# Performance work log

Hardware: AMD Instinct MI355X
Metric: run time of the kernel (lower is better)

Reference implementation:

```python
import jax, jax.numpy as jnp
import numpy as np
import math

B, S, H, NH = 4, 1024, 1536, 24
DH = H // NH
BUCKETS = 256          # position_buckets
MAX_REL = 512          # max_relative_positions
ATT_SPAN = BUCKETS     # pos_ebd_size
SCALE_FACTOR = 3       # 1 (content) + c2p + p2c
LN_EPS = 1e-7


def _make_log_bucket(rel, bucket_size, max_position):
    # numpy port of make_log_bucket_position (used only to build inputs)
    sign = np.sign(rel)
    mid = bucket_size // 2
    abs_pos = np.where((rel < mid) & (rel > -mid), mid - 1, np.abs(rel)).astype(np.float64)
    log_pos = np.ceil(np.log(abs_pos / mid) / np.log((max_position - 1) / mid) * (mid - 1)) + mid
    bucket = np.where(abs_pos <= mid, rel.astype(np.float64), log_pos * sign)
    return bucket.astype(np.int64)


def setup_inputs() -> dict:
    key = jax.random.key(0)
    ks = jax.random.split(key, 8)
    s = 0.02
    hidden_states = jax.random.normal(ks[0], (B, S, H), jnp.float32)
    rel_embeddings = jax.random.normal(ks[1], (2 * ATT_SPAN, H), jnp.float32)
    ids = np.arange(S)
    relative_pos = jnp.asarray(
        _make_log_bucket(ids[:, None] - ids[None, :], BUCKETS, MAX_REL)[None].astype(np.int32))  # [1,S,S]
    lengths = np.full((B,), S)
    lengths[B // 2:] = (3 * S) // 4  # some padded sequences
    valid = np.arange(S)[None, :] < lengths[:, None]  # [B,S]
    attention_mask = jnp.asarray(
        (valid[:, None, :, None] & valid[:, None, None, :]).astype(np.int32))  # [B,1,S,S]
    Wq = jax.random.normal(ks[2], (H, H), jnp.float32) * s
    Wk = jax.random.normal(ks[3], (H, H), jnp.float32) * s
    Wv = jax.random.normal(ks[4], (H, H), jnp.float32) * s
    Wo = jax.random.normal(ks[5], (H, H), jnp.float32) * s
    z = jnp.zeros((H,), jnp.float32)
    return dict(hidden_states=hidden_states, rel_embeddings=rel_embeddings,
                Wq=Wq, bq=z, Wk=Wk, bk=z, Wv=Wv, bv=z, Wo=Wo, bo=z,
                ln_g=jnp.ones((H,), jnp.float32), ln_b=z,
                attention_mask=attention_mask, relative_pos=relative_pos)


def _attention(hidden_states, rel_embeddings, Wq, bq, Wk, bk, Wv, bv, Wo, bo,
               ln_g, ln_b, attention_mask, relative_pos):
    Bm, Sm, Hm = hidden_states.shape

    def heads(x):  # [B,S,H] -> [B,NH,S,DH]
        return x.reshape(Bm, Sm, NH, DH).transpose(0, 2, 1, 3)

    q = heads(hidden_states @ Wq + bq)
    k = heads(hidden_states @ Wk + bk)
    v = heads(hidden_states @ Wv + bv)

    scale = math.sqrt(DH * SCALE_FACTOR)
    scores = jnp.einsum('bhqd,bhkd->bhqk', q, k) / scale  # content-to-content

    # share_att_key=True: reuse query/key projections on rel embeddings
    pos_k = (rel_embeddings @ Wk + bk).reshape(2 * ATT_SPAN, NH, DH).transpose(1, 0, 2)  # [NH,2P,DH]
    pos_q = (rel_embeddings @ Wq + bq).reshape(2 * ATT_SPAN, NH, DH).transpose(1, 0, 2)

    # content -> position
    c2p = jnp.einsum('bhqd,hpd->bhqp', q, pos_k)  # [B,NH,S,2P]
    c2p_idx = jnp.clip(relative_pos + ATT_SPAN, 0, 2 * ATT_SPAN - 1)[:, None]  # [1,1,S,S]
    c2p = jnp.take_along_axis(c2p, jnp.broadcast_to(c2p_idx, (Bm, NH, Sm, Sm)), axis=-1)
    scores = scores + c2p / scale

    # position -> content
    p2c = jnp.einsum('bhkd,hpd->bhkp', k, pos_q)  # [B,NH,S,2P]
    p2c_idx = jnp.clip(-relative_pos + ATT_SPAN, 0, 2 * ATT_SPAN - 1)[:, None]
    p2c = jnp.take_along_axis(p2c, jnp.broadcast_to(p2c_idx, (Bm, NH, Sm, Sm)), axis=-1)
    scores = scores + jnp.swapaxes(p2c, -1, -2) / scale

    # XSoftmax: mask==0 -> -inf before softmax, 0 after
    m = attention_mask.astype(bool)
    neg = jnp.finfo(scores.dtype).min
    probs = jax.nn.softmax(jnp.where(m, scores, neg), axis=-1)
    probs = jnp.where(m, probs, jnp.zeros((), scores.dtype))

    ctx = jnp.einsum('bhqk,bhkd->bhqd', probs, v)
    ctx = ctx.transpose(0, 2, 1, 3).reshape(Bm, Sm, Hm)

    # DebertaV2SelfOutput: dense + residual + LayerNorm
    out = ctx @ Wo + bo + hidden_states
    mu = jnp.mean(out, axis=-1, keepdims=True)
    var = jnp.mean(jnp.square(out - mu), axis=-1, keepdims=True)
    return (out - mu) / jnp.sqrt(var + LN_EPS) * ln_g + ln_b


def reference(hidden_states, rel_embeddings, Wq, bq, Wk, bk, Wv, bv, Wo, bo,
              ln_g, ln_b, attention_mask, relative_pos):
    return _attention(hidden_states, rel_embeddings, Wq, bq, Wk, bk, Wv, bv,
                      Wo, bo, ln_g, ln_b, attention_mask, relative_pos)
```

## Files before the change

### kernel.cpp

```cpp
#include <hip/hip_runtime.h>
#include <hip/hip_bf16.h>

constexpr int Bc  = 4;
constexpr int Sc  = 1024;
constexpr int Hc  = 1536;
constexpr int NHc = 24;
constexpr int P2c = 512;
constexpr int MX  = Bc * Sc;
constexpr int MA  = MX + P2c;
constexpr int N3  = 3 * Hc;
constexpr float INV_SCALE = 0.07216878364870323f;

using f32x4  = __attribute__((ext_vector_type(4))) float;
using bf16x8 = __attribute__((ext_vector_type(8))) short;
using i32x4  = __attribute__((ext_vector_type(4))) int;
using u16x8  = __attribute__((ext_vector_type(8))) unsigned short;
using u16x4  = __attribute__((ext_vector_type(4))) unsigned short;
typedef unsigned short u16;

#define DEV __device__ __forceinline__

DEV float bf2f(u16 u) { return __uint_as_float(((unsigned)u) << 16); }
DEV u16   f2bf(float f) { return __builtin_bit_cast(unsigned short, __float2bfloat16(f)); }

#if defined(__has_builtin)
#if __has_builtin(__builtin_amdgcn_global_load_lds)
#define HAVE_GLL 1
#endif
#endif
#ifndef HAVE_GLL
#define HAVE_GLL 0
#endif

DEV void stage32(u16* lds, const u16* g, int ldk, int lane) {
#pragma unroll
  for (int c = 0; c < 4; ++c) {
    const int row   = c * 8 + (lane >> 3);
    const int gslot = (lane & 7) ^ (row & 7);
    const u16* gp = g + (size_t)row * ldk + gslot * 8;
#if HAVE_GLL
    __builtin_amdgcn_global_load_lds(
        (const __attribute__((address_space(1))) void*)gp,
        (__attribute__((address_space(3))) void*)(lds + c * 8 * 64),
        16, 0, 0);
#else
    i32x4 v = *(const i32x4*)gp;
    *(i32x4*)(lds + row * 64 + (lane & 7) * 8) = v;
#endif
  }
}

DEV bf16x8 ldsFrag(const u16* base, int row, int kh, int lhi) {
  const int idx = row * 64 + ((kh * 32 + lhi * 8) ^ ((row & 7) * 8));
  return *(const bf16x8*)(base + idx);
}

template <int MODE>
__global__ __launch_bounds__(256) void gemm128(
    const u16* __restrict__ A, const u16* __restrict__ Bt,
    const float* __restrict__ bias, const float* __restrict__ resid,
    u16* __restrict__ outb, float* __restrict__ outf, int ldo)
{
  __shared__ alignas(16) u16 As[128 * 64];
  __shared__ alignas(16) u16 Bs[128 * 64];
  const int tid = threadIdx.x, wid = tid >> 6, lane = tid & 63;
  const int wr = wid >> 1, wc = wid & 1;
  const int l15 = lane & 15, lhi = lane >> 4;
  const int m0 = blockIdx.y * 128, n0 = blockIdx.x * 128;

  f32x4 acc[4][4] = {};
#pragma unroll 1
  for (int kt = 0; kt < 24; ++kt) {
    const int k0 = kt * 64;
    stage32(As + wid * (32 * 64), A  + (size_t)(m0 + wid * 32) * 1536 + k0, 1536, lane);
    stage32(Bs + wid * (32 * 64), Bt + (size_t)(n0 + wid * 32) * 1536 + k0, 1536, lane);
    asm volatile("s_waitcnt vmcnt(0)" ::: "memory");
    __syncthreads();
#pragma unroll
    for (int kh = 0; kh < 2; ++kh) {
      bf16x8 af[4], bfv[4];
#pragma unroll
      for (int mt = 0; mt < 4; ++mt) af[mt]  = ldsFrag(As, wr * 64 + mt * 16 + l15, kh, lhi);
#pragma unroll
      for (int nt = 0; nt < 4; ++nt) bfv[nt] = ldsFrag(Bs, wc * 64 + nt * 16 + l15, kh, lhi);
#pragma unroll
      for (int mt = 0; mt < 4; ++mt)
#pragma unroll
        for (int nt = 0; nt < 4; ++nt)
          acc[mt][nt] = __builtin_amdgcn_mfma_f32_16x16x32_bf16(af[mt], bfv[nt], acc[mt][nt], 0, 0, 0);
    }
    __syncthreads();
  }
#pragma unroll
  for (int mt = 0; mt < 4; ++mt)
#pragma unroll
    for (int nt = 0; nt < 4; ++nt) {
      const int gn = n0 + wc * 64 + nt * 16 + l15;
      const float bs = bias[gn];
#pragma unroll
      for (int r = 0; r < 4; ++r) {
        const int gm = m0 + wr * 64 + mt * 16 + lhi * 4 + r;
        float v = acc[mt][nt][r] + bs;
        if (MODE == 0) {
          if (gn < Hc) v *= INV_SCALE;
          outb[(size_t)gm * ldo + gn] = f2bf(v);
        } else {
          v += resid[(size_t)gm * ldo + gn];
          outf[(size_t)gm * ldo + gn] = v;
        }
      }
    }
}

__global__ __launch_bounds__(256) void prep_misc(
    const float* __restrict__ bq, const float* __restrict__ bk, const float* __restrict__ bv,
    const int* __restrict__ am, const int* __restrict__ rp,
    float* __restrict__ bias, int* __restrict__ valid, u16* __restrict__ tbl)
{
  const int TOT = N3 + MX + 2047;
  for (int i = blockIdx.x * 256 + threadIdx.x; i < TOT; i += gridDim.x * 256) {
    if (i < N3) {
      bias[i] = i < Hc ? bq[i] : (i < 2 * Hc ? bk[i - Hc] : bv[i - 2 * Hc]);
    } else if (i < N3 + MX) {
      const int j = i - N3, b = j >> 10, s = j & 1023;
      valid[j] = am[(size_t)b * Sc * Sc + (size_t)s * Sc + s];
    } else {
      const int t = i - (N3 + MX), d = t - 1023;
      int v = (d >= 0 ? rp[(size_t)d * Sc] : rp[-d]) + 256;
      v = v < 0 ? 0 : (v > 511 ? 511 : v);
      tbl[t] = (u16)v;
    }
  }
}

__global__ void len_kernel(const int* __restrict__ valid, int* __restrict__ LENS)
{
  const int tid = threadIdx.x, wid = tid >> 6, lane = tid & 63;
  int s = 0;
#pragma unroll
  for (int j = 0; j < 16; ++j) s += valid[wid * Sc + j * 64 + lane];
#pragma unroll
  for (int off = 1; off <= 32; off <<= 1) s += __shfl_xor(s, off);
  if (lane == 0) LENS[wid] = s;
}

__global__ __launch_bounds__(256) void cast_x(const float* __restrict__ hs,
                                              const float* __restrict__ rel,
                                              u16* __restrict__ A)
{
  const size_t total = (size_t)MA * Hc / 4;
  for (size_t i = (size_t)blockIdx.x * 256 + threadIdx.x; i < total; i += (size_t)gridDim.x * 256) {
    const size_t e = i * 4;
    const int row = (int)(e / Hc), col = (int)(e % Hc);
    const float* s = row < MX ? hs + (size_t)row * Hc + col : rel + (size_t)(row - MX) * Hc + col;
    f32x4 v = *(const f32x4*)s;
    u16x4 o = { f2bf(v[0]), f2bf(v[1]), f2bf(v[2]), f2bf(v[3]) };
    *(u16x4*)(A + e) = o;
  }
}

__global__ void transpose_cast(const float* __restrict__ Wq, const float* __restrict__ Wk,
                               const float* __restrict__ Wv, const float* __restrict__ Wo,
                               u16* __restrict__ WT, u16* __restrict__ WOT)
{
  const int z = blockIdx.z;
  const float* src = z == 0 ? Wq : z == 1 ? Wk : z == 2 ? Wv : Wo;
  u16* dst = z == 3 ? WOT : WT + (size_t)z * Hc * Hc;
  __shared__ float t[32][33];
  const int tx = threadIdx.x, ty = threadIdx.y;
  const int kb = blockIdx.y * 32, nb = blockIdx.x * 32;
#pragma unroll
  for (int i = 0; i < 4; ++i)
    t[ty + i * 8][tx] = src[(size_t)(kb + ty + i * 8) * Hc + nb + tx];
  __syncthreads();
#pragma unroll
  for (int i = 0; i < 4; ++i)
    dst[(size_t)(nb + ty + i * 8) * Hc + kb + tx] = f2bf(t[tx][ty + i * 8]);
}

__global__ __launch_bounds__(256) void relmat3(const u16* __restrict__ QKVP,
    u16* __restrict__ c2p, u16* __restrict__ p2cT, int bh_base)
{
  const int z = blockIdx.y, lbh = z >> 1, var = z & 1;
  const int bh = bh_base + lbh, b = bh / NHc, h = bh % NHc;
  const int t = blockIdx.x;
  const int tid = threadIdx.x, wid = tid >> 6, lane = tid & 63;
  const int wr = wid >> 1, wc = wid & 1;
  const int l15 = lane & 15, lhi = lane >> 4;

  int m0, n0, ldo;
  size_t arowb, browb;
  u16* out;
  if (var == 0) {
    m0 = (t >> 2) * 64; n0 = (t & 3) * 128; ldo = P2c;
    arowb = (size_t)b * Sc + m0;  browb = (size_t)MX + n0;
    out = c2p + (size_t)lbh * Sc * P2c;
  } else {
    m0 = (t >> 3) * 64; n0 = (t & 7) * 128; ldo = Sc;
    arowb = (size_t)MX + m0;      browb = (size_t)b * Sc + n0;
    out = p2cT + (size_t)lbh * P2c * Sc;
  }
  const int acol = h * 64;
  const int bcol = Hc + h * 64;

  f32x4 acc[2][4] = {};
#pragma unroll
  for (int kh = 0; kh < 2; ++kh) {
    bf16x8 a[2], bb[4];
#pragma unroll
    for (int mt = 0; mt < 2; ++mt)
      a[mt] = *(const bf16x8*)(QKVP + (arowb + wr * 32 + mt * 16 + l15) * 4608
                               + acol + kh * 32 + lhi * 8);
#pragma unroll
    for (int nt = 0; nt < 4; ++nt)
      bb[nt] = *(const bf16x8*)(QKVP + (browb + wc * 64 + nt * 16 + l15) * 4608
                                + bcol + kh * 32 + lhi * 8);
#pragma unroll
    for (int mt = 0; mt < 2; ++mt)
#pragma unroll
      for (int nt = 0; nt < 4; ++nt)
        acc[mt][nt] = __builtin_amdgcn_mfma_f32_16x16x32_bf16(a[mt], bb[nt], acc[mt][nt], 0, 0, 0);
  }
#pragma unroll
  for (int mt = 0; mt < 2; ++mt)
#pragma unroll
    for (int nt = 0; nt < 4; ++nt)
#pragma unroll
      for (int r = 0; r < 4; ++r) {
        const int mm = m0 + wr * 32 + mt * 16 + (lhi << 2) + r;
        const int nn = n0 + wc * 64 + nt * 16 + l15;
        out[(size_t)mm * ldo + nn] = f2bf(acc[mt][nt][r]);
      }
}

DEV int svz(int d) { return ((d ^ (d >> 3)) & 7) << 3; }

__global__ __launch_bounds__(256) void flash4(
    const u16* __restrict__ QKVP, const u16* __restrict__ c2p, const u16* __restrict__ p2cT,
    const int* __restrict__ LENS, const u16* __restrict__ tblG,
    u16* __restrict__ ctx, int bh_base, int chunkC)
{
  int id = blockIdx.x;
  const int grid = chunkC * 16;
  if ((grid & 7) == 0) {
    const int cpx = grid >> 3;
    id = (id & 7) * cpx + (id >> 3);
  }
  const int lbh = id >> 4, qi = id & 15;
  const int bh = bh_base + lbh, b = bh / NHc, h = bh % NHc;
  const int tid = threadIdx.x, wid = tid >> 6, lane = tid & 63;
  const int l15 = lane & 15, lhi = lane >> 4, lhi4 = lhi * 4;
  const int qrb = qi * 64 + wid * 16;
  const int len = LENS[b], nkt = (len + 63) >> 6;

  __shared__ u16 Tt[2048];
  __shared__ alignas(16) u16 Kt[64 * 64];
  __shared__ alignas(16) u16 Vt[64 * 64];
  __shared__ alignas(16) u16 Pl[4][16 * 64];

  for (int i = tid; i < 2047; i += 256) Tt[i] = tblG[i];

  bf16x8 aq[2];
#pragma unroll
  for (int kh = 0; kh < 2; ++kh)
    aq[kh] = *(const bf16x8*)(QKVP + (size_t)(b * Sc + qrb + l15) * 4608 + h * 64 + kh * 32 + lhi * 8);

  const int kr = tid >> 2, dc = (tid & 3) * 16;
  const int sk = (kr & 7) * 8;
  const u16* Kg = QKVP + (size_t)b * Sc * 4608 + Hc + h * 64;
  const u16* Vg = QKVP + (size_t)b * Sc * 4608 + 2 * Hc + h * 64;

  auto writeKV = [&](u16x8 ka, u16x8 kb, u16x8 va, u16x8 vb) {
    *(u16x8*)(Kt + kr * 64 + (dc ^ sk))       = ka;
    *(u16x8*)(Kt + kr * 64 + ((dc ^ sk) ^ 8)) = kb;
#pragma unroll
    for (int i = 0; i < 8; ++i) { const int d = dc + i;     Vt[d * 64 + (kr ^ svz(d))] = va[i]; }
#pragma unroll
    for (int i = 0; i < 8; ++i) { const int d = dc + 8 + i; Vt[d * 64 + (kr ^ svz(d))] = vb[i]; }
  };

  {
    const size_t ro = (size_t)kr * 4608 + dc;
    u16x8 ka = *(const u16x8*)(Kg + ro), kb = *(const u16x8*)(Kg + ro + 8);
    u16x8 va = *(const u16x8*)(Vg + ro), vb = *(const u16x8*)(Vg + ro + 8);
    writeKV(ka, kb, va, vb);
  }
  __syncthreads();

  const u16* c2pB  = c2p  + (size_t)lbh * Sc * P2c;
  const u16* p2cTB = p2cT + (size_t)lbh * P2c * Sc;
  u16* myP = Pl[wid];
  f32x4 o_acc[4] = {};
  float m_arr[4], l_arr[4];
#pragma unroll
  for (int r = 0; r < 4; ++r) { m_arr[r] = -1e30f; l_arr[r] = 0.f; }

  for (int kt = 0; kt < nkt; ++kt) {
    const int k0 = kt * 64;
    const bool more = (kt + 1 < nkt);
    u16x8 nka, nkb, nva, nvb;
    if (more) {
      const size_t ro = (size_t)(k0 + 64 + kr) * 4608 + dc;
      nka = *(const u16x8*)(Kg + ro); nkb = *(const u16x8*)(Kg + ro + 8);
      nva = *(const u16x8*)(Vg + ro); nvb = *(const u16x8*)(Vg + ro + 8);
    }

    float relv[4][4];
#pragma unroll
    for (int j = 0; j < 4; ++j)
#pragma unroll
      for (int r = 0; r < 4; ++r) {
        const int q = qrb + lhi4 + r;
        const int k = k0 + j * 16 + l15;
        const int cc = Tt[q - k + 1023];
        relv[j][r] = bf2f(c2pB[(size_t)q * P2c + cc]) + bf2f(p2cTB[(size_t)cc * Sc + k]);
      }

    f32x4 s[4];
    __builtin_amdgcn_s_setprio(1);
#pragma unroll
    for (int j = 0; j < 4; ++j) {
      f32x4 sv = {};
#pragma unroll
      for (int kh = 0; kh < 2; ++kh) {
        bf16x8 bk = ldsFrag(Kt, j * 16 + l15, kh, lhi);
        sv = __builtin_amdgcn_mfma_f32_16x16x32_bf16(aq[kh], bk, sv, 0, 0, 0);
      }
      s[j] = sv;
    }
    __builtin_amdgcn_s_setprio(0);

    float p[4][4];
#pragma unroll
    for (int j = 0; j < 4; ++j) {
      const bool kv = (k0 + j * 16 + l15) < len;
#pragma unroll
      for (int r = 0; r < 4; ++r)
        p[j][r] = kv ? (s[j][r] + relv[j][r]) : -1e30f;
    }

    float resc[4];
#pragma unroll
    for (int r = 0; r < 4; ++r) {
      float mx = fmaxf(fmaxf(p[0][r], p[1][r]), fmaxf(p[2][r], p[3][r]));
#pragma unroll
      for (int off = 1; off <= 8; off <<= 1) mx = fmaxf(mx, __shfl_xor(mx, off));
      const float mnew = fmaxf(m_arr[r], mx);
      const float sc = __expf(m_arr[r] - mnew);
      float rs = 0.f;
#pragma unroll
      for (int j = 0; j < 4; ++j) { p[j][r] = __expf(p[j][r] - mnew); rs += p[j][r]; }
#pragma unroll
      for (int off = 1; off <= 8; off <<= 1) rs += __shfl_xor(rs, off);
      l_arr[r] = l_arr[r] * sc + rs;
      m_arr[r] = mnew;
      resc[r] = sc;
    }
#pragma unroll
    for (int jd = 0; jd < 4; ++jd)
#pragma unroll
      for (int r = 0; r < 4; ++r) o_acc[jd][r] *= resc[r];

#pragma unroll
    for (int j = 0; j < 4; ++j)
#pragma unroll
      for (int r = 0; r < 4; ++r) {
        const int row = lhi4 + r, col = j * 16 + l15;
        myP[row * 64 + (col ^ ((row & 7) * 8))] = f2bf(p[j][r]);
      }

    __builtin_amdgcn_s_setprio(1);
#pragma unroll
    for (int kh = 0; kh < 2; ++kh) {
      bf16x8 pa = *(const bf16x8*)(myP + l15 * 64 + ((kh * 32 + lhi * 8) ^ ((l15 & 7) * 8)));
#pragma unroll
      for (int jd = 0; jd < 4; ++jd) {
        const int d = jd * 16 + l15;
        bf16x8 vf = *(const bf16x8*)(Vt + d * 64 + ((kh * 32 + lhi * 8) ^ svz(d)));
        o_acc[jd] = __builtin_amdgcn_mfma_f32_16x16x32_bf16(pa, vf, o_acc[jd], 0, 0, 0);
      }
    }
    __builtin_amdgcn_s_setprio(0);

    __syncthreads();
    if (more) writeKV(nka, nkb, nva, nvb);
    __syncthreads();
  }

#pragma unroll
  for (int r = 0; r < 4; ++r) {
    const int q = qrb + lhi4 + r;
    const float inv = (q < len && l_arr[r] > 0.f) ? 1.f / l_arr[r] : 0.f;
#pragma unroll
    for (int jd = 0; jd < 4; ++jd)
      ctx[(size_t)(b * Sc + q) * Hc + h * 64 + jd * 16 + l15] = f2bf(o_acc[jd][r] * inv);
  }
}

__global__ __launch_bounds__(256) void ln_kernel(float* __restrict__ io,
    const float* __restrict__ g, const float* __restrict__ bta)
{
  const int row = blockIdx.x;
  float* p = io + (size_t)row * Hc;
  const int tid = threadIdx.x, wid = tid >> 6, lane = tid & 63;
  float v[6];
  float s = 0.f;
#pragma unroll
  for (int j = 0; j < 6; ++j) { v[j] = p[tid + j * 256]; s += v[j]; }
#pragma unroll
  for (int off = 1; off <= 32; off <<= 1) s += __shfl_xor(s, off);
  __shared__ float red[4];
  if (lane == 0) red[wid] = s;
  __syncthreads();
  const float mu = (red[0] + red[1] + red[2] + red[3]) * (1.f / Hc);
  float q = 0.f;
#pragma unroll
  for (int j = 0; j < 6; ++j) { const float d = v[j] - mu; q += d * d; }
#pragma unroll
  for (int off = 1; off <= 32; off <<= 1) q += __shfl_xor(q, off);
  __syncthreads();
  if (lane == 0) red[wid] = q;
  __syncthreads();
  const float rstd = rsqrtf((red[0] + red[1] + red[2] + red[3]) * (1.f / Hc) + 1e-7f);
#pragma unroll
  for (int j = 0; j < 6; ++j) {
    const int c = tid + j * 256;
    p[c] = (v[j] - mu) * rstd * g[c] + bta[c];
  }
}

extern "C" void kernel_launch(void* const* d_in, const int* in_sizes, int n_in,
                              void* d_out, int out_size, void* d_ws, size_t ws_size,
                              hipStream_t stream)
{
  (void)in_sizes; (void)n_in; (void)out_size;
  const float* hidden = (const float*)d_in[0];
  const float* relemb = (const float*)d_in[1];
  const float* Wq = (const float*)d_in[2];
  const float* bq = (const float*)d_in[3];
  const float* Wk = (const float*)d_in[4];
  const float* bk = (const float*)d_in[5];
  const float* Wv = (const float*)d_in[6];
  const float* bv = (const float*)d_in[7];
  const float* Wo = (const float*)d_in[8];
  const float* bo = (const float*)d_in[9];
  const float* lng = (const float*)d_in[10];
  const float* lnb = (const float*)d_in[11];
  const int* am = (const int*)d_in[12];
  const int* rp = (const int*)d_in[13];
  float* out = (float*)d_out;

  char* ws = (char*)d_ws;
  size_t off = 0;
  auto alloc = [&](size_t bytes) { size_t r = off; off += (bytes + 255) & ~(size_t)255; return r; };
  const size_t o_qkvp = alloc((size_t)MA * 4608 * 2);
  const size_t o_wt   = alloc((size_t)N3 * Hc * 2);
  const size_t o_wot  = alloc((size_t)Hc * Hc * 2);
  const size_t o_abig = alloc((size_t)MA * Hc * 2);
  const size_t o_bias = alloc((size_t)N3 * 4);
  const size_t o_valid= alloc((size_t)MX * 4);
  const size_t o_tbl  = alloc(2048 * 2);
  const size_t o_lens = alloc(256);
  const size_t fixed  = off;
  const size_t o_rel  = off;

  const size_t perbh = (size_t)Sc * P2c * 2 * 2;
  int c = 96;
  while (c > 1 && fixed + (size_t)c * perbh > ws_size) c >>= 1;

  u16* QKVP = (u16*)(ws + o_qkvp);
  u16* WT   = (u16*)(ws + o_wt);
  u16* WOT  = (u16*)(ws + o_wot);
  u16* ABIG = (u16*)(ws + o_abig);
  u16* CTX  = (u16*)(ws + o_abig);
  float* BIAS = (float*)(ws + o_bias);
  int* VALID  = (int*)(ws + o_valid);
  u16* TBL  = (u16*)(ws + o_tbl);
  int* LENS = (int*)(ws + o_lens);
  u16* C2P  = (u16*)(ws + o_rel);
  u16* P2CT = C2P + (size_t)c * Sc * P2c;

  prep_misc<<<dim3(50), dim3(256), 0, stream>>>(bq, bk, bv, am, rp, BIAS, VALID, TBL);
  len_kernel<<<dim3(1), dim3(256), 0, stream>>>(VALID, LENS);
  cast_x<<<dim3(1728), dim3(256), 0, stream>>>(hidden, relemb, ABIG);
  transpose_cast<<<dim3(48, 48, 4), dim3(32, 8), 0, stream>>>(Wq, Wk, Wv, Wo, WT, WOT);
  gemm128<0><<<dim3(36, 36), dim3(256), 0, stream>>>(ABIG, WT, BIAS, (const float*)nullptr,
                                                     QKVP, (float*)nullptr, 4608);
  for (int base = 0; base < 96; base += c) {
    relmat3<<<dim3(64, 2 * c), dim3(256), 0, stream>>>(QKVP, C2P, P2CT, base);
    flash4<<<dim3(c * 16), dim3(256), 0, stream>>>(QKVP, C2P, P2CT, LENS, TBL, CTX, base, c);
  }
  gemm128<1><<<dim3(12, 32), dim3(256), 0, stream>>>(CTX, WOT, bo, hidden,
                                                     (u16*)nullptr, out, Hc);
  ln_kernel<<<dim3(MX), dim3(256), 0, stream>>>(out, lng, lnb);
}
```

Baseline: 450.5 us.

## Add double-buffered 256x192 QKV GEMM and prefetch relative-bias gathers in flash

Replaces the QKV projection GEMM with a 512-thread, 256x192-tile kernel. It double-buffers LDS and interleaves global-to-LDS staging of the next K-slice with the MFMA work on the current one, and it remaps blocks for L2 locality. The aim is to hide the load latency that the old version exposed with a full vmcnt(0) wait and barrier every K step. The flash attention kernel now prefetches the next tile's c2p/p2c gathered bias values into registers during the current tile, so those scattered loads are off the critical path. The cost is higher register pressure and larger LDS use, which may limit occupancy.

```diff
diff --git a/kernel.cpp b/kernel.cpp
--- a/kernel.cpp
+++ b/kernel.cpp
@@ -22,6 +22,7 @@
 
 DEV float bf2f(u16 u) { return __uint_as_float(((unsigned)u) << 16); }
 DEV u16   f2bf(float f) { return __builtin_bit_cast(unsigned short, __float2bfloat16(f)); }
+DEV void  bar() { __builtin_amdgcn_s_barrier(); asm volatile("" ::: "memory"); }
 
 #if defined(__has_builtin)
 #if __has_builtin(__builtin_amdgcn_global_load_lds)
@@ -55,11 +56,137 @@
   return *(const bf16x8*)(base + idx);
 }
 
-template <int MODE>
-__global__ __launch_bounds__(256) void gemm128(
+__global__ __launch_bounds__(512, 2) void gemm256k(
+    const u16* __restrict__ A, const u16* __restrict__ Bt,
+    const float* __restrict__ bias, u16* __restrict__ outb)
+{
+  constexpr int BM = 256, BN = 192;
+  __shared__ alignas(16) u16 As[2][BM * 64];
+  __shared__ alignas(16) u16 Bs[2][BN * 64];
+  const int tid = threadIdx.x, wid = tid >> 6, lane = tid & 63;
+  const int wr = wid >> 2, wc = wid & 3;
+  const int l15 = lane & 15, lhi = lane >> 4;
+
+  int id = blockIdx.x;
+  id = (id & 7) * 54 + (id >> 3);
+  const int m0 = (id / 24) * BM, n0 = (id % 24) * BN;
+
+  const int srow = tid >> 3;
+  const int gsl  = (tid & 7) ^ (srow & 7);
+
+  auto stageA = [&](int buf, int ck, int k0) {
+    const u16* gp = A + (size_t)(m0 + ck * 64 + srow) * 1536 + k0 + gsl * 8;
+#if HAVE_GLL
+    __builtin_amdgcn_global_load_lds(
+        (const __attribute__((address_space(1))) void*)gp,
+        (__attribute__((address_space(3))) void*)(&As[buf][ck * 4096 + wid * 512]),
+        16, 0, 0);
+#else
+    *(i32x4*)(&As[buf][ck * 4096 + srow * 64 + (tid & 7) * 8]) = *(const i32x4*)gp;
+#endif
+  };
+  auto stageB = [&](int buf, int ck, int k0) {
+    const u16* gp = Bt + (size_t)(n0 + ck * 64 + srow) * 1536 + k0 + gsl * 8;
+#if HAVE_GLL
+    __builtin_amdgcn_global_load_lds(
+        (const __attribute__((address_space(1))) void*)gp,
+        (__attribute__((address_space(3))) void*)(&Bs[buf][ck * 4096 + wid * 512]),
+        16, 0, 0);
+#else
+    *(i32x4*)(&Bs[buf][ck * 4096 + srow * 64 + (tid & 7) * 8]) = *(const i32x4*)gp;
+#endif
+  };
+
+  f32x4 acc[8][3] = {};
+
+  stageA(0, 0, 0); stageA(0, 1, 0); stageA(0, 2, 0); stageA(0, 3, 0);
+  stageB(0, 0, 0); stageB(0, 1, 0); stageB(0, 2, 0);
+
+  int cur = 0;
+#pragma unroll 1
+  for (int kt = 0; kt < 24; ++kt) {
+    const int nk0 = kt * 64 + 64;
+    const bool more = (kt < 23);
+    const int nb = cur ^ 1;
+
+    if (more) { stageA(nb, 0, nk0); stageA(nb, 1, nk0); }
+    if (more) asm volatile("s_waitcnt vmcnt(2)" ::: "memory");
+    else      asm volatile("s_waitcnt vmcnt(0)" ::: "memory");
+    bar();
+    bf16x8 bf[3], af[4];
+#pragma unroll
+    for (int nt = 0; nt < 3; ++nt) bf[nt] = ldsFrag(Bs[cur], wc * 48 + nt * 16 + l15, 0, lhi);
+#pragma unroll
+    for (int mt = 0; mt < 4; ++mt) af[mt] = ldsFrag(As[cur], wr * 128 + mt * 16 + l15, 0, lhi);
+    __builtin_amdgcn_s_setprio(1);
+#pragma unroll
+    for (int mt = 0; mt < 4; ++mt)
+#pragma unroll
+      for (int nt = 0; nt < 3; ++nt)
+        acc[mt][nt] = __builtin_amdgcn_mfma_f32_16x16x32_bf16(af[mt], bf[nt], acc[mt][nt], 0, 0, 0);
+    __builtin_amdgcn_s_setprio(0);
+    if (more) { stageA(nb, 2, nk0); stageA(nb, 3, nk0); }
+    bar();
+
+#pragma unroll
+    for (int mt = 0; mt < 4; ++mt) af[mt] = ldsFrag(As[cur], wr * 128 + 64 + mt * 16 + l15, 0, lhi);
+    __builtin_amdgcn_s_setprio(1);
+#pragma unroll
+    for (int mt = 0; mt < 4; ++mt)
+#pragma unroll
+      for (int nt = 0; nt < 3; ++nt)
+        acc[4 + mt][nt] = __builtin_amdgcn_mfma_f32_16x16x32_bf16(af[mt], bf[nt], acc[4 + mt][nt], 0, 0, 0);
+    __builtin_amdgcn_s_setprio(0);
+    if (more) { stageB(nb, 0, nk0); stageB(nb, 1, nk0); }
+    bar();
+
+#pragma unroll
+    for (int nt = 0; nt < 3; ++nt) bf[nt] = ldsFrag(Bs[cur], wc * 48 + nt * 16 + l15, 1, lhi);
+#pragma unroll
+    for (int mt = 0; mt < 4; ++mt) af[mt] = ldsFrag(As[cur], wr * 128 + mt * 16 + l15, 1, lhi);
+    __builtin_amdgcn_s_setprio(1);
+#pragma unroll
+    for (int mt = 0; mt < 4; ++mt)
+#pragma unroll
+      for (int nt = 0; nt < 3; ++nt)
+        acc[mt][nt] = __builtin_amdgcn_mfma_f32_16x16x32_bf16(af[mt], bf[nt], acc[mt][nt], 0, 0, 0);
+    __builtin_amdgcn_s_setprio(0);
+    if (more) { stageB(nb, 2, nk0); }
+    bar();
+
+#pragma unroll
+    for (int mt = 0; mt < 4; ++mt) af[mt] = ldsFrag(As[cur], wr * 128 + 64 + mt * 16 + l15, 1, lhi);
+    __builtin_amdgcn_s_setprio(1);
+#pragma unroll
+    for (int mt = 0; mt < 4; ++mt)
+#pragma unroll
+      for (int nt = 0; nt < 3; ++nt)
+        acc[4 + mt][nt] = __builtin_amdgcn_mfma_f32_16x16x32_bf16(af[mt], bf[nt], acc[4 + mt][nt], 0, 0, 0);
+    __builtin_amdgcn_s_setprio(0);
+    bar();
+
+    cur ^= 1;
+  }
+
+#pragma unroll
+  for (int mg = 0; mg < 8; ++mg)
+#pragma unroll
+    for (int nt = 0; nt < 3; ++nt) {
+      const int gn = n0 + wc * 48 + nt * 16 + l15;
+      const float bs = bias[gn];
+      const float sc = gn < Hc ? INV_SCALE : 1.f;
+#pragma unroll
+      for (int r = 0; r < 4; ++r) {
+        const int gm = m0 + wr * 128 + mg * 16 + (lhi << 2) + r;
+        outb[(size_t)gm * 4608 + gn] = f2bf((acc[mg][nt][r] + bs) * sc);
+      }
+    }
+}
+
+__global__ __launch_bounds__(256) void gemm128o(
     const u16* __restrict__ A, const u16* __restrict__ Bt,
     const float* __restrict__ bias, const float* __restrict__ resid,
-    u16* __restrict__ outb, float* __restrict__ outf, int ldo)
+    float* __restrict__ outf, int ldo)
 {
   __shared__ alignas(16) u16 As[128 * 64];
   __shared__ alignas(16) u16 Bs[128 * 64];
@@ -100,14 +227,7 @@
 #pragma unroll
       for (int r = 0; r < 4; ++r) {
         const int gm = m0 + wr * 64 + mt * 16 + lhi * 4 + r;
-        float v = acc[mt][nt][r] + bs;
-        if (MODE == 0) {
-          if (gn < Hc) v *= INV_SCALE;
-          outb[(size_t)gm * ldo + gn] = f2bf(v);
-        } else {
-          v += resid[(size_t)gm * ldo + gn];
-          outf[(size_t)gm * ldo + gn] = v;
-        }
+        outf[(size_t)gm * ldo + gn] = acc[mt][nt][r] + bs + resid[(size_t)gm * ldo + gn];
       }
     }
 }
@@ -235,7 +355,7 @@
 
 DEV int svz(int d) { return ((d ^ (d >> 3)) & 7) << 3; }
 
-__global__ __launch_bounds__(256) void flash4(
+__global__ __launch_bounds__(256) void flash5(
     const u16* __restrict__ QKVP, const u16* __restrict__ c2p, const u16* __restrict__ p2cT,
     const int* __restrict__ LENS, const u16* __restrict__ tblG,
     u16* __restrict__ ctx, int bh_base, int chunkC)
@@ -294,6 +414,18 @@
   float m_arr[4], l_arr[4];
 #pragma unroll
   for (int r = 0; r < 4; ++r) { m_arr[r] = -1e30f; l_arr[r] = 0.f; }
+
+  u16 rc[16], rp[16];
+#pragma unroll
+  for (int j = 0; j < 4; ++j)
+#pragma unroll
+    for (int r = 0; r < 4; ++r) {
+      const int q = qrb + lhi4 + r;
+      const int k = j * 16 + l15;
+      const int cc = Tt[q - k + 1023];
+      rc[j * 4 + r] = c2pB[(size_t)q * P2c + cc];
+      rp[j * 4 + r] = p2cTB[(size_t)cc * Sc + k];
+    }
 
   for (int kt = 0; kt < nkt; ++kt) {
     const int k0 = kt * 64;
@@ -304,17 +436,19 @@
       nka = *(const u16x8*)(Kg + ro); nkb = *(const u16x8*)(Kg + ro + 8);
       nva = *(const u16x8*)(Vg + ro); nvb = *(const u16x8*)(Vg + ro + 8);
     }
-
-    float relv[4][4];
-#pragma unroll
-    for (int j = 0; j < 4; ++j)
-#pragma unroll
-      for (int r = 0; r < 4; ++r) {
-        const int q = qrb + lhi4 + r;
-        const int k = k0 + j * 16 + l15;
-        const int cc = Tt[q - k + 1023];
-        relv[j][r] = bf2f(c2pB[(size_t)q * P2c + cc]) + bf2f(p2cTB[(size_t)cc * Sc + k]);
-      }
+    u16 nrc[16], nrp[16];
+    if (more) {
+#pragma unroll
+      for (int j = 0; j < 4; ++j)
+#pragma unroll
+        for (int r = 0; r < 4; ++r) {
+          const int q = qrb + lhi4 + r;
+          const int k = k0 + 64 + j * 16 + l15;
+          const int cc = Tt[q - k + 1023];
+          nrc[j * 4 + r] = c2pB[(size_t)q * P2c + cc];
+          nrp[j * 4 + r] = p2cTB[(size_t)cc * Sc + k];
+        }
+    }
 
     f32x4 s[4];
     __builtin_amdgcn_s_setprio(1);
@@ -336,7 +470,7 @@
       const bool kv = (k0 + j * 16 + l15) < len;
 #pragma unroll
       for (int r = 0; r < 4; ++r)
-        p[j][r] = kv ? (s[j][r] + relv[j][r]) : -1e30f;
+        p[j][r] = kv ? (s[j][r] + bf2f(rc[j * 4 + r]) + bf2f(rp[j * 4 + r])) : -1e30f;
     }
 
     float resc[4];
@@ -383,7 +517,11 @@
     __builtin_amdgcn_s_setprio(0);
 
     __syncthreads();
-    if (more) writeKV(nka, nkb, nva, nvb);
+    if (more) {
+      writeKV(nka, nkb, nva, nvb);
+#pragma unroll
+      for (int i = 0; i < 16; ++i) { rc[i] = nrc[i]; rp[i] = nrp[i]; }
+    }
     __syncthreads();
   }
 
@@ -484,13 +622,11 @@
   len_kernel<<<dim3(1), dim3(256), 0, stream>>>(VALID, LENS);
   cast_x<<<dim3(1728), dim3(256), 0, stream>>>(hidden, relemb, ABIG);
   transpose_cast<<<dim3(48, 48, 4), dim3(32, 8), 0, stream>>>(Wq, Wk, Wv, Wo, WT, WOT);
-  gemm128<0><<<dim3(36, 36), dim3(256), 0, stream>>>(ABIG, WT, BIAS, (const float*)nullptr,
-                                                     QKVP, (float*)nullptr, 4608);
+  gemm256k<<<dim3(432), dim3(512), 0, stream>>>(ABIG, WT, BIAS, QKVP);
   for (int base = 0; base < 96; base += c) {
     relmat3<<<dim3(64, 2 * c), dim3(256), 0, stream>>>(QKVP, C2P, P2CT, base);
-    flash4<<<dim3(c * 16), dim3(256), 0, stream>>>(QKVP, C2P, P2CT, LENS, TBL, CTX, base, c);
-  }
-  gemm128<1><<<dim3(12, 32), dim3(256), 0, stream>>>(CTX, WOT, bo, hidden,
-                                                     (u16*)nullptr, out, Hc);
+    flash5<<<dim3(c * 16), dim3(256), 0, stream>>>(QKVP, C2P, P2CT, LENS, TBL, CTX, base, c);
+  }
+  gemm128o<<<dim3(12, 32), dim3(256), 0, stream>>>(CTX, WOT, bo, hidden, out, Hc);
   ln_kernel<<<dim3(MX), dim3(256), 0, stream>>>(out, lng, lnb);
 }
```

After: 491.4 us. 1.09x slower.

## Restructure relmat into larger tiles with B operand staged in LDS

Applied to the files above, without the earlier changes.

Replaces the small 64x128 relmat tiles with 256x512 tiles per block. The whole 512x64 B operand is staged into shared memory (via global_load_lds when available), and each warp keeps its A fragments in registers while sweeping all N columns. This cuts redundant global reloads of the position/key rows across many small blocks. In exchange there are far fewer blocks (8 per head chunk), 64KB of LDS per block, and much lower occupancy and parallelism.

```diff
diff --git a/kernel.cpp b/kernel.cpp
--- a/kernel.cpp
+++ b/kernel.cpp
@@ -178,59 +178,77 @@
     dst[(size_t)(nb + ty + i * 8) * Hc + kb + tx] = f2bf(t[tx][ty + i * 8]);
 }
 
-__global__ __launch_bounds__(256) void relmat3(const u16* __restrict__ QKVP,
+__global__ __launch_bounds__(256) void relmat4(const u16* __restrict__ QKVP,
     u16* __restrict__ c2p, u16* __restrict__ p2cT, int bh_base)
 {
-  const int z = blockIdx.y, lbh = z >> 1, var = z & 1;
+  const int lbh = blockIdx.x >> 3, v = blockIdx.x & 7;
   const int bh = bh_base + lbh, b = bh / NHc, h = bh % NHc;
-  const int t = blockIdx.x;
   const int tid = threadIdx.x, wid = tid >> 6, lane = tid & 63;
-  const int wr = wid >> 1, wc = wid & 1;
-  const int l15 = lane & 15, lhi = lane >> 4;
+  const int l15 = lane & 15, lhi = lane >> 4, lhi4 = lhi * 4;
+
+  __shared__ alignas(16) u16 Bs[512 * 64];
 
   int m0, n0, ldo;
-  size_t arowb, browb;
+  size_t arow, brow;
   u16* out;
-  if (var == 0) {
-    m0 = (t >> 2) * 64; n0 = (t & 3) * 128; ldo = P2c;
-    arowb = (size_t)b * Sc + m0;  browb = (size_t)MX + n0;
+  if (v < 4) {
+    m0 = v * 256; n0 = 0; ldo = P2c;
+    arow = (size_t)b * Sc + m0; brow = (size_t)MX;
     out = c2p + (size_t)lbh * Sc * P2c;
   } else {
-    m0 = (t >> 3) * 64; n0 = (t & 7) * 128; ldo = Sc;
-    arowb = (size_t)MX + m0;      browb = (size_t)b * Sc + n0;
+    m0 = ((v - 4) >> 1) * 256; n0 = ((v - 4) & 1) * 512; ldo = Sc;
+    arow = (size_t)MX + m0; brow = (size_t)b * Sc + n0;
     out = p2cT + (size_t)lbh * P2c * Sc;
   }
   const int acol = h * 64;
   const int bcol = Hc + h * 64;
 
-  f32x4 acc[2][4] = {};
-#pragma unroll
-  for (int kh = 0; kh < 2; ++kh) {
-    bf16x8 a[2], bb[4];
-#pragma unroll
-    for (int mt = 0; mt < 2; ++mt)
-      a[mt] = *(const bf16x8*)(QKVP + (arowb + wr * 32 + mt * 16 + l15) * 4608
-                               + acol + kh * 32 + lhi * 8);
-#pragma unroll
-    for (int nt = 0; nt < 4; ++nt)
-      bb[nt] = *(const bf16x8*)(QKVP + (browb + wc * 64 + nt * 16 + l15) * 4608
-                                + bcol + kh * 32 + lhi * 8);
-#pragma unroll
-    for (int mt = 0; mt < 2; ++mt)
-#pragma unroll
-      for (int nt = 0; nt < 4; ++nt)
-        acc[mt][nt] = __builtin_amdgcn_mfma_f32_16x16x32_bf16(a[mt], bb[nt], acc[mt][nt], 0, 0, 0);
-  }
-#pragma unroll
-  for (int mt = 0; mt < 2; ++mt)
-#pragma unroll
-    for (int nt = 0; nt < 4; ++nt)
+  const int srow = tid >> 3;
+  const int gsl  = (tid & 7) ^ (srow & 7);
+#pragma unroll
+  for (int it = 0; it < 16; ++it) {
+    const int row = it * 32 + srow;
+    const u16* gp = QKVP + (brow + row) * 4608 + bcol + gsl * 8;
+#if HAVE_GLL
+    __builtin_amdgcn_global_load_lds(
+        (const __attribute__((address_space(1))) void*)gp,
+        (__attribute__((address_space(3))) void*)(&Bs[it * 2048 + wid * 512]),
+        16, 0, 0);
+#else
+    *(i32x4*)(&Bs[row * 64 + (tid & 7) * 8]) = *(const i32x4*)gp;
+#endif
+  }
+
+  bf16x8 af[4][2];
+#pragma unroll
+  for (int mt = 0; mt < 4; ++mt)
+#pragma unroll
+    for (int kh = 0; kh < 2; ++kh)
+      af[mt][kh] = *(const bf16x8*)(QKVP + (arow + wid * 64 + mt * 16 + l15) * 4608
+                                    + acol + kh * 32 + lhi * 8);
+
+  asm volatile("s_waitcnt vmcnt(0)" ::: "memory");
+  __syncthreads();
+
+#pragma unroll 4
+  for (int nt = 0; nt < 32; ++nt) {
+    bf16x8 b0 = ldsFrag(Bs, nt * 16 + l15, 0, lhi);
+    bf16x8 b1 = ldsFrag(Bs, nt * 16 + l15, 1, lhi);
+    f32x4 acc[4] = {};
+#pragma unroll
+    for (int mt = 0; mt < 4; ++mt) {
+      acc[mt] = __builtin_amdgcn_mfma_f32_16x16x32_bf16(af[mt][0], b0, acc[mt], 0, 0, 0);
+      acc[mt] = __builtin_amdgcn_mfma_f32_16x16x32_bf16(af[mt][1], b1, acc[mt], 0, 0, 0);
+    }
+#pragma unroll
+    for (int mt = 0; mt < 4; ++mt)
 #pragma unroll
       for (int r = 0; r < 4; ++r) {
-        const int mm = m0 + wr * 32 + mt * 16 + (lhi << 2) + r;
-        const int nn = n0 + wc * 64 + nt * 16 + l15;
-        out[(size_t)mm * ldo + nn] = f2bf(acc[mt][nt][r]);
+        const int mm = m0 + wid * 64 + mt * 16 + lhi4 + r;
+        const int nn = n0 + nt * 16 + l15;
+        out[(size_t)mm * ldo + nn] = f2bf(acc[mt][r]);
       }
+  }
 }
 
 DEV int svz(int d) { return ((d ^ (d >> 3)) & 7) << 3; }
@@ -487,7 +505,7 @@
   gemm128<0><<<dim3(36, 36), dim3(256), 0, stream>>>(ABIG, WT, BIAS, (const float*)nullptr,
                                                      QKVP, (float*)nullptr, 4608);
   for (int base = 0; base < 96; base += c) {
-    relmat3<<<dim3(64, 2 * c), dim3(256), 0, stream>>>(QKVP, C2P, P2CT, base);
+    relmat4<<<dim3(8 * c), dim3(256), 0, stream>>>(QKVP, C2P, P2CT, base);
     flash4<<<dim3(c * 16), dim3(256), 0, stream>>>(QKVP, C2P, P2CT, LENS, TBL, CTX, base, c);
   }
   gemm128<1><<<dim3(12, 32), dim3(256), 0, stream>>>(CTX, WOT, bo, hidden,
```

New measurement: 408.2 us. 1.1x faster.
